# Performance work log

Hardware: AMD Instinct MI355X
Metric: run time of the kernel (lower is better)

## Reference

```python
import jax, jax.numpy as jnp
import numpy as np

EPS = 1e-5
NEG = -1.0e9

def ln(x, g, b):
    m = x.mean(-1, keepdims=True)
    v = ((x - m) ** 2).mean(-1, keepdims=True)
    return (x - m) * jax.lax.rsqrt(v + EPS) * g + b

def setup_inputs() -> dict:
    B, N, DH, DE, H = 2, 512, 256, 64, 8
    key = jax.random.key(0)
    ks = jax.random.split(key, 8)
    s = 0.02
    f32 = jnp.float32
    return {
        'h': jax.random.normal(ks[0], (B, N, DH), f32),
        'e': jax.random.normal(ks[1], (B, N, N, DE), f32),
        'mask': jnp.ones((B, N), f32),
        'Wqkv': jax.random.normal(ks[2], (DH, 3 * DH), f32) * s,
        'bqkv': jnp.zeros((3 * DH,), f32),
        'Wout': jax.random.normal(ks[3], (DH, DH), f32) * s,
        'bout': jnp.zeros((DH,), f32),
        'Web': jax.random.normal(ks[4], (DE, H), f32) * s,
        'beb': jnp.zeros((H,), f32),
        'eb_g': jnp.ones((H,), f32), 'eb_b': jnp.zeros((H,), f32),
        'W1': jax.random.normal(ks[5], (2 * DH + DE, DE), f32) * s,
        'b1': jnp.zeros((DE,), f32),
        'mlp_g': jnp.ones((DE,), f32), 'mlp_b': jnp.zeros((DE,), f32),
        'W2': jax.random.normal(ks[6], (DE, DE), f32) * s,
        'b2': jnp.zeros((DE,), f32),
        'nh_g': jnp.ones((DH,), f32), 'nh_b': jnp.zeros((DH,), f32),
        'ne_g': jnp.ones((DE,), f32), 'ne_b': jnp.zeros((DE,), f32),
    }

def reference(h, e, mask, Wqkv, bqkv, Wout, bout, Web, beb, eb_g, eb_b,
              W1, b1, mlp_g, mlp_b, W2, b2, nh_g, nh_b, ne_g, ne_b):
    B, N, DH = h.shape
    DE = e.shape[-1]
    H = Web.shape[-1]
    dh = DH // H
    # additive pad mask: [B,N,N] -> broadcast over heads
    pad = (1.0 - mask) * NEG                  # [B,N]
    attn_mask = (pad[:, :, None] + pad[:, None, :])[:, None]  # [B,1,N,N]
    h_res = h
    hn = ln(h, nh_g, nh_b)
    qkv = hn @ Wqkv + bqkv                    # [B,N,3*DH]
    q, k, v = jnp.split(qkv, 3, axis=-1)
    q = q.reshape(B, N, H, dh)
    k = k.reshape(B, N, H, dh)
    v = v.reshape(B, N, H, dh)
    en = ln(e, ne_g, ne_b)                    # [B,N,N,DE]
    edge_bias = ln(en @ Web + beb, eb_g, eb_b)  # [B,N,N,H]
    edge_bias = jnp.transpose(edge_bias, (0, 3, 1, 2))  # [B,H,N,N]
    scores = jnp.einsum('bihd,bjhd->bhij', q, k) / np.sqrt(dh).astype(np.float32)
    probs = jax.nn.softmax(scores + edge_bias + attn_mask, axis=-1)
    h_out = jnp.einsum('bhij,bjhd->bihd', probs, v).reshape(B, N, DH)
    h_out = h_out @ Wout + bout
    h_new = h_res + h_out                     # dropout p=0 (eval)
    # pairwise edge update
    h_i = jnp.broadcast_to(h_new[:, :, None, :], (B, N, N, DH))
    h_j = jnp.broadcast_to(h_new[:, None, :, :], (B, N, N, DH))
    e_in = jnp.concatenate([h_i, h_j, en], axis=-1)  # [B,N,N,2*DH+DE]
    e_out = ln(jax.nn.relu(e_in @ W1 + b1), mlp_g, mlp_b) @ W2 + b2
    e_new = e + e_out
    return (h_new, e_new)
```

## Files before the change

### kernel.cpp

```cpp
#include <hip/hip_runtime.h>
#include <math.h>

#define BB 2
#define NN 512
#define DH 256
#define DE 64
#define NH 8
#define EPS 1e-5f
#define NEGV (-1.0e9f)

__global__ __launch_bounds__(256) void k1_ln_qkv(
    const float* __restrict__ h, const float* __restrict__ nh_g,
    const float* __restrict__ nh_b, const float* __restrict__ Wqkv,
    const float* __restrict__ bqkv, float* __restrict__ q,
    float* __restrict__ k, float* __restrict__ vt)
{
    __shared__ float hn[4][DH];
    const int tid = threadIdx.x;
    const int wave = tid >> 6, lane = tid & 63;
    const int row0 = blockIdx.x * 4;
    const int row = row0 + wave;

    float x[4];
    float s = 0.f, ss = 0.f;
#pragma unroll
    for (int jj = 0; jj < 4; jj++) {
        x[jj] = h[(size_t)row * DH + lane + 64 * jj];
        s += x[jj]; ss += x[jj] * x[jj];
    }
#pragma unroll
    for (int m = 32; m >= 1; m >>= 1) { s += __shfl_xor(s, m); ss += __shfl_xor(ss, m); }
    const float mean = s * (1.0f / DH);
    const float var = ss * (1.0f / DH) - mean * mean;
    const float rstd = rsqrtf(var + EPS);
#pragma unroll
    for (int jj = 0; jj < 4; jj++) {
        const int c = lane + 64 * jj;
        hn[wave][c] = (x[jj] - mean) * rstd * nh_g[c] + nh_b[c];
    }
    __syncthreads();

    float acc[4][3];
#pragma unroll
    for (int r = 0; r < 4; r++) {
        acc[r][0] = bqkv[tid];
        acc[r][1] = bqkv[tid + 256];
        acc[r][2] = bqkv[tid + 512];
    }
    for (int kk = 0; kk < DH; kk++) {
        const float w0 = Wqkv[(size_t)kk * 768 + tid];
        const float w1 = Wqkv[(size_t)kk * 768 + tid + 256];
        const float w2 = Wqkv[(size_t)kk * 768 + tid + 512];
#pragma unroll
        for (int r = 0; r < 4; r++) {
            const float hv = hn[r][kk];
            acc[r][0] += hv * w0; acc[r][1] += hv * w1; acc[r][2] += hv * w2;
        }
    }
    const float qscale = 0.17677669529663687f;
    const int hh = tid >> 5, d = tid & 31;
#pragma unroll
    for (int r = 0; r < 4; r++) {
        const int rw = row0 + r;
        const int b = rw >> 9, i = rw & 511;
        q[(((size_t)(b * NH + hh) * NN) + i) * 32 + d] = acc[r][0] * qscale;
        k[(((size_t)(b * NH + hh) * NN) + i) * 32 + d] = acc[r][1];
        vt[(((size_t)(b * NH + hh) * 32) + d) * NN + i] = acc[r][2];
    }
}

__global__ __launch_bounds__(256) void k2_edge_bias(
    const float* __restrict__ e, const float* __restrict__ Web,
    const float* __restrict__ beb, const float* __restrict__ eb_g,
    const float* __restrict__ eb_b, const float* __restrict__ ne_g,
    const float* __restrict__ ne_b, float* __restrict__ ebias)
{
    __shared__ float tile[4][64][65];
    const int wave = threadIdx.x >> 6, lane = threadIdx.x & 63;
    const int t = blockIdx.x * 4 + wave;
    const int j0 = (t & 7) * 64;
    const int bi = t >> 3;
    const int b = bi >> 9, i = bi & 511;

    const float* src = e + ((size_t)bi * NN + j0) * DE;
#pragma unroll
    for (int it = 0; it < 16; it++) {
        const int f = it * 256 + lane * 4;
        const float4 v = *(const float4*)(src + f);
        const int r = f >> 6, c = f & 63;
        tile[wave][r][c] = v.x; tile[wave][r][c + 1] = v.y;
        tile[wave][r][c + 2] = v.z; tile[wave][r][c + 3] = v.w;
    }
    __syncthreads();

    float s = 0.f, ss = 0.f;
    for (int d = 0; d < 64; d++) {
        const float x = tile[wave][lane][d];
        s += x; ss += x * x;
    }
    const float mean = s * (1.0f / 64), var = ss * (1.0f / 64) - mean * mean;
    const float rstd = rsqrtf(var + EPS);

    float acc[8];
#pragma unroll
    for (int hh = 0; hh < 8; hh++) acc[hh] = beb[hh];
    for (int d = 0; d < 64; d++) {
        const float x = tile[wave][lane][d];
        const float en = (x - mean) * rstd * ne_g[d] + ne_b[d];
#pragma unroll
        for (int hh = 0; hh < 8; hh++) acc[hh] += en * Web[d * 8 + hh];
    }
    float s2 = 0.f, ss2 = 0.f;
#pragma unroll
    for (int hh = 0; hh < 8; hh++) { s2 += acc[hh]; ss2 += acc[hh] * acc[hh]; }
    const float m2 = s2 * 0.125f, v2 = ss2 * 0.125f - m2 * m2;
    const float r2 = rsqrtf(v2 + EPS);
#pragma unroll
    for (int hh = 0; hh < 8; hh++) {
        const float v = (acc[hh] - m2) * r2 * eb_g[hh] + eb_b[hh];
        ebias[(((size_t)(b * NH + hh) * NN) + i) * NN + j0 + lane] = v;
    }
}

__global__ __launch_bounds__(256) void k3a_softmax(
    const float* __restrict__ q, const float* __restrict__ k,
    const float* __restrict__ mask, float* __restrict__ ebias)
{
    const int bh = blockIdx.x >> 9;
    const int i = blockIdx.x & 511;
    const int b = bh >> 3;
    const int tid = threadIdx.x;
    const int wave = tid >> 6, lane = tid & 63;

    __shared__ __align__(16) float qrow[32];
    __shared__ float red[4];
    if (tid < 32) qrow[tid] = q[((size_t)bh * NN + i) * 32 + tid];
    __syncthreads();

    const float pad_i = (1.0f - mask[b * NN + i]) * NEGV;
    float sv[2];
#pragma unroll
    for (int u = 0; u < 2; u++) {
        const int j = tid + u * 256;
        const float4* kr = (const float4*)(k + ((size_t)bh * NN + j) * 32);
        float a = 0.f;
#pragma unroll
        for (int d4 = 0; d4 < 8; d4++) {
            const float4 kv = kr[d4];
            const float4 qv = *(const float4*)(qrow + d4 * 4);
            a += kv.x * qv.x + kv.y * qv.y + kv.z * qv.z + kv.w * qv.w;
        }
        const float pad_j = (1.0f - mask[b * NN + j]) * NEGV;
        sv[u] = a + ebias[(((size_t)bh * NN) + i) * NN + j] + pad_i + pad_j;
    }
    float mx = fmaxf(sv[0], sv[1]);
#pragma unroll
    for (int m = 32; m >= 1; m >>= 1) mx = fmaxf(mx, __shfl_xor(mx, m));
    if (lane == 0) red[wave] = mx;
    __syncthreads();
    mx = fmaxf(fmaxf(red[0], red[1]), fmaxf(red[2], red[3]));
    __syncthreads();
    const float p0 = __expf(sv[0] - mx), p1 = __expf(sv[1] - mx);
    float sm = p0 + p1;
#pragma unroll
    for (int m = 32; m >= 1; m >>= 1) sm += __shfl_xor(sm, m);
    if (lane == 0) red[wave] = sm;
    __syncthreads();
    const float inv = 1.0f / (red[0] + red[1] + red[2] + red[3]);
    ebias[(((size_t)bh * NN) + i) * NN + tid] = p0 * inv;
    ebias[(((size_t)bh * NN) + i) * NN + tid + 256] = p1 * inv;
}

__global__ __launch_bounds__(256) void k3b_av_out(
    const float* __restrict__ probs, const float* __restrict__ vt,
    const float* __restrict__ h, const float* __restrict__ Wout,
    const float* __restrict__ bout, float* __restrict__ hnew)
{
    const int bi = blockIdx.x;
    const int b = bi >> 9, i = bi & 511;
    const int tid = threadIdx.x;
    __shared__ __align__(16) float p[NH * NN];
    __shared__ float ao[DH];
#pragma unroll
    for (int it = 0; it < 16; it++) {
        const int f = it * 256 + tid;
        const int hh = f >> 9, j = f & 511;
        p[f] = probs[(((size_t)(b * NH + hh) * NN) + i) * NN + j];
    }
    __syncthreads();
    const int hh = tid >> 5, d = tid & 31;
    const float* vrow = vt + (((size_t)(b * NH + hh) * 32) + d) * NN;
    float a = 0.f;
    for (int j4 = 0; j4 < 128; j4++) {
        const float4 vv = *(const float4*)(vrow + j4 * 4);
        const float4 pv = *(const float4*)(&p[hh * NN + j4 * 4]);
        a += vv.x * pv.x + vv.y * pv.y + vv.z * pv.z + vv.w * pv.w;
    }
    ao[tid] = a;
    __syncthreads();
    float out = bout[tid];
    for (int kk = 0; kk < DH; kk++) out += ao[kk] * Wout[(size_t)kk * DH + tid];
    hnew[(size_t)bi * DH + tid] = h[(size_t)bi * DH + tid] + out;
}

__global__ __launch_bounds__(64) void k4_hw1(
    const float* __restrict__ hnew, const float* __restrict__ W1,
    const float* __restrict__ b1, float* __restrict__ hW1a,
    float* __restrict__ hW1b)
{
    const int row = blockIdx.x;
    const int c = threadIdx.x;
    __shared__ float hr[DH];
#pragma unroll
    for (int t = 0; t < 4; t++) hr[c + 64 * t] = hnew[(size_t)row * DH + c + 64 * t];
    __syncthreads();
    float a = b1[c], bb = 0.f;
    for (int kk = 0; kk < DH; kk++) {
        const float hv = hr[kk];
        a += hv * W1[(size_t)kk * 64 + c];
        bb += hv * W1[(size_t)(256 + kk) * 64 + c];
    }
    hW1a[(size_t)row * 64 + c] = a;
    hW1b[(size_t)row * 64 + c] = bb;
}

__global__ __launch_bounds__(256) void k5_edge_mlp(
    const float* __restrict__ e, const float* __restrict__ ne_g,
    const float* __restrict__ ne_b, const float* __restrict__ W1c,
    const float* __restrict__ hW1a, const float* __restrict__ hW1b,
    const float* __restrict__ mlp_g, const float* __restrict__ mlp_b,
    const float* __restrict__ W2, const float* __restrict__ b2,
    float* __restrict__ enew)
{
    __shared__ float tile[4][64][65];
    const int wave = threadIdx.x >> 6, lane = threadIdx.x & 63;
    const int t = blockIdx.x * 4 + wave;
    const int j0 = (t & 7) * 64;
    const int bi = t >> 3;
    const int b = bi >> 9;

    const float* src = e + ((size_t)bi * NN + j0) * DE;
#pragma unroll
    for (int it = 0; it < 16; it++) {
        const int f = it * 256 + lane * 4;
        const float4 v = *(const float4*)(src + f);
        const int r = f >> 6, c = f & 63;
        tile[wave][r][c] = v.x; tile[wave][r][c + 1] = v.y;
        tile[wave][r][c + 2] = v.z; tile[wave][r][c + 3] = v.w;
    }
    __syncthreads();

    float s = 0.f, ss = 0.f;
    for (int d = 0; d < 64; d++) {
        const float x = tile[wave][lane][d];
        s += x; ss += x * x;
    }
    const float mean = s * (1.0f / 64), var = ss * (1.0f / 64) - mean * mean;
    const float rstd = rsqrtf(var + EPS);
    for (int d = 0; d < 64; d++) {
        const float x = tile[wave][lane][d];
        tile[wave][lane][d] = (x - mean) * rstd * ne_g[d] + ne_b[d];
    }

    const float* hA = hW1a + (size_t)bi * 64;
    const float* hB = hW1b + ((size_t)(b * NN + j0 + lane)) * 64;
    float acc[64];
#pragma unroll
    for (int c4 = 0; c4 < 16; c4++) {
        const float4 ha = *(const float4*)(hA + c4 * 4);
        const float4 hb = *(const float4*)(hB + c4 * 4);
        acc[c4 * 4 + 0] = ha.x + hb.x; acc[c4 * 4 + 1] = ha.y + hb.y;
        acc[c4 * 4 + 2] = ha.z + hb.z; acc[c4 * 4 + 3] = ha.w + hb.w;
    }
    for (int d = 0; d < 64; d++) {
        const float en = tile[wave][lane][d];
        const float* w = W1c + (size_t)d * 64;
#pragma unroll
        for (int c = 0; c < 64; c++) acc[c] += en * w[c];
    }
    float s2 = 0.f, ss2 = 0.f;
#pragma unroll
    for (int c = 0; c < 64; c++) {
        acc[c] = fmaxf(acc[c], 0.f);
        s2 += acc[c]; ss2 += acc[c] * acc[c];
    }
    const float m2 = s2 * (1.0f / 64), v2 = ss2 * (1.0f / 64) - m2 * m2;
    const float r2 = rsqrtf(v2 + EPS);
#pragma unroll
    for (int c = 0; c < 64; c++)
        tile[wave][lane][c] = (acc[c] - m2) * r2 * mlp_g[c] + mlp_b[c];
#pragma unroll
    for (int c = 0; c < 64; c++) acc[c] = b2[c];
    for (int d = 0; d < 64; d++) {
        const float u = tile[wave][lane][d];
        const float* w = W2 + (size_t)d * 64;
#pragma unroll
        for (int c = 0; c < 64; c++) acc[c] += u * w[c];
    }
    const float* erow = e + (((size_t)bi * NN) + j0 + lane) * DE;
    float* drow = enew + (((size_t)bi * NN) + j0 + lane) * DE;
#pragma unroll
    for (int c4 = 0; c4 < 16; c4++) {
        const float4 ev = *(const float4*)(erow + c4 * 4);
        float4 o;
        o.x = acc[c4 * 4 + 0] + ev.x; o.y = acc[c4 * 4 + 1] + ev.y;
        o.z = acc[c4 * 4 + 2] + ev.z; o.w = acc[c4 * 4 + 3] + ev.w;
        *(float4*)(drow + c4 * 4) = o;
    }
}

extern "C" void kernel_launch(void* const* d_in, const int* in_sizes, int n_in,
                              void* d_out, int out_size, void* d_ws, size_t ws_size,
                              hipStream_t stream)
{
    const float* h    = (const float*)d_in[0];
    const float* e    = (const float*)d_in[1];
    const float* mask = (const float*)d_in[2];
    const float* Wqkv = (const float*)d_in[3];
    const float* bqkv = (const float*)d_in[4];
    const float* Wout = (const float*)d_in[5];
    const float* bout = (const float*)d_in[6];
    const float* Web  = (const float*)d_in[7];
    const float* beb  = (const float*)d_in[8];
    const float* eb_g = (const float*)d_in[9];
    const float* eb_b = (const float*)d_in[10];
    const float* W1   = (const float*)d_in[11];
    const float* b1   = (const float*)d_in[12];
    const float* mlp_g= (const float*)d_in[13];
    const float* mlp_b= (const float*)d_in[14];
    const float* W2   = (const float*)d_in[15];
    const float* b2   = (const float*)d_in[16];
    const float* nh_g = (const float*)d_in[17];
    const float* nh_b = (const float*)d_in[18];
    const float* ne_g = (const float*)d_in[19];
    const float* ne_b = (const float*)d_in[20];

    float* ws   = (float*)d_ws;
    float* q    = ws;
    float* kbuf = ws + 262144;
    float* vt   = ws + 524288;
    float* eb   = ws + 786432;
    float* hW1a = ws + 786432 + 4194304;
    float* hW1b = hW1a + 65536;

    float* hnew = (float*)d_out;
    float* enew = hnew + 262144;

    hipLaunchKernelGGL(k1_ln_qkv, dim3(256), dim3(256), 0, stream,
                       h, nh_g, nh_b, Wqkv, bqkv, q, kbuf, vt);
    hipLaunchKernelGGL(k2_edge_bias, dim3(2048), dim3(256), 0, stream,
                       e, Web, beb, eb_g, eb_b, ne_g, ne_b, eb);
    hipLaunchKernelGGL(k3a_softmax, dim3(8192), dim3(256), 0, stream,
                       q, kbuf, mask, eb);
    hipLaunchKernelGGL(k3b_av_out, dim3(1024), dim3(256), 0, stream,
                       eb, vt, h, Wout, bout, hnew);
    hipLaunchKernelGGL(k4_hw1, dim3(1024), dim3(64), 0, stream,
                       hnew, W1, b1, hW1a, hW1b);
    hipLaunchKernelGGL(k5_edge_mlp, dim3(2048), dim3(256), 0, stream,
                       e, ne_g, ne_b, W1 + 512 * 64, hW1a, hW1b,
                       mlp_g, mlp_b, W2, b2, enew);
}
```

Before: 687.3 us.

## Drop LDS edge tiles; read edge rows directly per thread and keep MLP in registers

The edge-bias and edge-MLP kernels no longer stage the 64-wide edge rows through a padded shared-memory tile. Each thread now reads its own row straight from global memory with float4 loads, twice (once for LayerNorm statistics, once for the projection), and the second MLP layer runs in two 32-column halves from register-resident activations instead of going through LDS. The output projection in the attention kernel is also split into four independent accumulators to shorten the dependency chain. Per-thread row loads are strided 256 bytes apart across lanes, so coalescing is worse and the edge tensor is read more times, with reliance on cache to absorb the repeats. Register pressure may also rise.

```diff
diff --git a/kernel.cpp b/kernel.cpp
--- a/kernel.cpp
+++ b/kernel.cpp
@@ -75,28 +75,18 @@
     const float* __restrict__ eb_b, const float* __restrict__ ne_g,
     const float* __restrict__ ne_b, float* __restrict__ ebias)
 {
-    __shared__ float tile[4][64][65];
-    const int wave = threadIdx.x >> 6, lane = threadIdx.x & 63;
-    const int t = blockIdx.x * 4 + wave;
-    const int j0 = (t & 7) * 64;
-    const int bi = t >> 3;
-    const int b = bi >> 9, i = bi & 511;
-
-    const float* src = e + ((size_t)bi * NN + j0) * DE;
-#pragma unroll
-    for (int it = 0; it < 16; it++) {
-        const int f = it * 256 + lane * 4;
-        const float4 v = *(const float4*)(src + f);
-        const int r = f >> 6, c = f & 63;
-        tile[wave][r][c] = v.x; tile[wave][r][c + 1] = v.y;
-        tile[wave][r][c + 2] = v.z; tile[wave][r][c + 3] = v.w;
-    }
-    __syncthreads();
+    const int idx = blockIdx.x * 256 + threadIdx.x;
+    const int b = idx >> 18;
+    const int i = (idx >> 9) & 511;
+    const int j = idx & 511;
+    const float4* erow = (const float4*)(e + (size_t)idx * DE);
 
     float s = 0.f, ss = 0.f;
-    for (int d = 0; d < 64; d++) {
-        const float x = tile[wave][lane][d];
-        s += x; ss += x * x;
+#pragma unroll 1
+    for (int d4 = 0; d4 < 16; d4++) {
+        const float4 v = erow[d4];
+        s += v.x + v.y + v.z + v.w;
+        ss += v.x * v.x + v.y * v.y + v.z * v.z + v.w * v.w;
     }
     const float mean = s * (1.0f / 64), var = ss * (1.0f / 64) - mean * mean;
     const float rstd = rsqrtf(var + EPS);
@@ -104,11 +94,20 @@
     float acc[8];
 #pragma unroll
     for (int hh = 0; hh < 8; hh++) acc[hh] = beb[hh];
-    for (int d = 0; d < 64; d++) {
-        const float x = tile[wave][lane][d];
-        const float en = (x - mean) * rstd * ne_g[d] + ne_b[d];
-#pragma unroll
-        for (int hh = 0; hh < 8; hh++) acc[hh] += en * Web[d * 8 + hh];
+#pragma unroll 1
+    for (int d4 = 0; d4 < 16; d4++) {
+        const float4 v = erow[d4];
+        float en[4];
+        en[0] = (v.x - mean) * rstd * ne_g[d4 * 4 + 0] + ne_b[d4 * 4 + 0];
+        en[1] = (v.y - mean) * rstd * ne_g[d4 * 4 + 1] + ne_b[d4 * 4 + 1];
+        en[2] = (v.z - mean) * rstd * ne_g[d4 * 4 + 2] + ne_b[d4 * 4 + 2];
+        en[3] = (v.w - mean) * rstd * ne_g[d4 * 4 + 3] + ne_b[d4 * 4 + 3];
+#pragma unroll
+        for (int t = 0; t < 4; t++) {
+            const float* w = Web + (d4 * 4 + t) * 8;
+#pragma unroll
+            for (int hh = 0; hh < 8; hh++) acc[hh] += en[t] * w[hh];
+        }
     }
     float s2 = 0.f, ss2 = 0.f;
 #pragma unroll
@@ -118,7 +117,7 @@
 #pragma unroll
     for (int hh = 0; hh < 8; hh++) {
         const float v = (acc[hh] - m2) * r2 * eb_g[hh] + eb_b[hh];
-        ebias[(((size_t)(b * NH + hh) * NN) + i) * NN + j0 + lane] = v;
+        ebias[(((size_t)(b * NH + hh) * NN) + i) * NN + j] = v;
     }
 }
 
@@ -198,9 +197,15 @@
     }
     ao[tid] = a;
     __syncthreads();
-    float out = bout[tid];
-    for (int kk = 0; kk < DH; kk++) out += ao[kk] * Wout[(size_t)kk * DH + tid];
-    hnew[(size_t)bi * DH + tid] = h[(size_t)bi * DH + tid] + out;
+    float o0 = 0.f, o1 = 0.f, o2 = 0.f, o3 = 0.f;
+    for (int kk = 0; kk < DH; kk += 4) {
+        o0 += ao[kk + 0] * Wout[(size_t)(kk + 0) * DH + tid];
+        o1 += ao[kk + 1] * Wout[(size_t)(kk + 1) * DH + tid];
+        o2 += ao[kk + 2] * Wout[(size_t)(kk + 2) * DH + tid];
+        o3 += ao[kk + 3] * Wout[(size_t)(kk + 3) * DH + tid];
+    }
+    hnew[(size_t)bi * DH + tid] =
+        h[(size_t)bi * DH + tid] + bout[tid] + ((o0 + o1) + (o2 + o3));
 }
 
 __global__ __launch_bounds__(64) void k4_hw1(
@@ -232,38 +237,24 @@
     const float* __restrict__ W2, const float* __restrict__ b2,
     float* __restrict__ enew)
 {
-    __shared__ float tile[4][64][65];
-    const int wave = threadIdx.x >> 6, lane = threadIdx.x & 63;
-    const int t = blockIdx.x * 4 + wave;
-    const int j0 = (t & 7) * 64;
-    const int bi = t >> 3;
-    const int b = bi >> 9;
-
-    const float* src = e + ((size_t)bi * NN + j0) * DE;
-#pragma unroll
-    for (int it = 0; it < 16; it++) {
-        const int f = it * 256 + lane * 4;
-        const float4 v = *(const float4*)(src + f);
-        const int r = f >> 6, c = f & 63;
-        tile[wave][r][c] = v.x; tile[wave][r][c + 1] = v.y;
-        tile[wave][r][c + 2] = v.z; tile[wave][r][c + 3] = v.w;
-    }
-    __syncthreads();
+    const int idx = blockIdx.x * 256 + threadIdx.x;
+    const int b = idx >> 18;
+    const int j = idx & 511;
+    const int bi = idx >> 9;
+    const float4* erow = (const float4*)(e + (size_t)idx * DE);
 
     float s = 0.f, ss = 0.f;
-    for (int d = 0; d < 64; d++) {
-        const float x = tile[wave][lane][d];
-        s += x; ss += x * x;
+#pragma unroll 1
+    for (int d4 = 0; d4 < 16; d4++) {
+        const float4 v = erow[d4];
+        s += v.x + v.y + v.z + v.w;
+        ss += v.x * v.x + v.y * v.y + v.z * v.z + v.w * v.w;
     }
     const float mean = s * (1.0f / 64), var = ss * (1.0f / 64) - mean * mean;
     const float rstd = rsqrtf(var + EPS);
-    for (int d = 0; d < 64; d++) {
-        const float x = tile[wave][lane][d];
-        tile[wave][lane][d] = (x - mean) * rstd * ne_g[d] + ne_b[d];
-    }
 
     const float* hA = hW1a + (size_t)bi * 64;
-    const float* hB = hW1b + ((size_t)(b * NN + j0 + lane)) * 64;
+    const float* hB = hW1b + ((size_t)(b * NN + j)) * 64;
     float acc[64];
 #pragma unroll
     for (int c4 = 0; c4 < 16; c4++) {
@@ -272,12 +263,23 @@
         acc[c4 * 4 + 0] = ha.x + hb.x; acc[c4 * 4 + 1] = ha.y + hb.y;
         acc[c4 * 4 + 2] = ha.z + hb.z; acc[c4 * 4 + 3] = ha.w + hb.w;
     }
-    for (int d = 0; d < 64; d++) {
-        const float en = tile[wave][lane][d];
-        const float* w = W1c + (size_t)d * 64;
-#pragma unroll
-        for (int c = 0; c < 64; c++) acc[c] += en * w[c];
-    }
+
+#pragma unroll 1
+    for (int d4 = 0; d4 < 16; d4++) {
+        const float4 v = erow[d4];
+        float en[4];
+        en[0] = (v.x - mean) * rstd * ne_g[d4 * 4 + 0] + ne_b[d4 * 4 + 0];
+        en[1] = (v.y - mean) * rstd * ne_g[d4 * 4 + 1] + ne_b[d4 * 4 + 1];
+        en[2] = (v.z - mean) * rstd * ne_g[d4 * 4 + 2] + ne_b[d4 * 4 + 2];
+        en[3] = (v.w - mean) * rstd * ne_g[d4 * 4 + 3] + ne_b[d4 * 4 + 3];
+#pragma unroll
+        for (int t = 0; t < 4; t++) {
+            const float* w = W1c + (size_t)(d4 * 4 + t) * 64;
+#pragma unroll
+            for (int c = 0; c < 64; c++) acc[c] += en[t] * w[c];
+        }
+    }
+
     float s2 = 0.f, ss2 = 0.f;
 #pragma unroll
     for (int c = 0; c < 64; c++) {
@@ -288,24 +290,30 @@
     const float r2 = rsqrtf(v2 + EPS);
 #pragma unroll
     for (int c = 0; c < 64; c++)
-        tile[wave][lane][c] = (acc[c] - m2) * r2 * mlp_g[c] + mlp_b[c];
-#pragma unroll
-    for (int c = 0; c < 64; c++) acc[c] = b2[c];
-    for (int d = 0; d < 64; d++) {
-        const float u = tile[wave][lane][d];
-        const float* w = W2 + (size_t)d * 64;
-#pragma unroll
-        for (int c = 0; c < 64; c++) acc[c] += u * w[c];
-    }
-    const float* erow = e + (((size_t)bi * NN) + j0 + lane) * DE;
-    float* drow = enew + (((size_t)bi * NN) + j0 + lane) * DE;
-#pragma unroll
-    for (int c4 = 0; c4 < 16; c4++) {
-        const float4 ev = *(const float4*)(erow + c4 * 4);
-        float4 o;
-        o.x = acc[c4 * 4 + 0] + ev.x; o.y = acc[c4 * 4 + 1] + ev.y;
-        o.z = acc[c4 * 4 + 2] + ev.z; o.w = acc[c4 * 4 + 3] + ev.w;
-        *(float4*)(drow + c4 * 4) = o;
+        acc[c] = (acc[c] - m2) * r2 * mlp_g[c] + mlp_b[c];
+
+    const float* erowf = e + (size_t)idx * 64;
+    float* drow = enew + (size_t)idx * 64;
+#pragma unroll
+    for (int half = 0; half < 2; half++) {
+        float outc[32];
+#pragma unroll
+        for (int c = 0; c < 32; c++) outc[c] = b2[half * 32 + c];
+#pragma unroll
+        for (int d = 0; d < 64; d++) {
+            const float u = acc[d];
+            const float* w = W2 + (size_t)d * 64 + half * 32;
+#pragma unroll
+            for (int c = 0; c < 32; c++) outc[c] += u * w[c];
+        }
+#pragma unroll
+        for (int c4 = 0; c4 < 8; c4++) {
+            const float4 ev = *(const float4*)(erowf + half * 32 + c4 * 4);
+            float4 o;
+            o.x = outc[c4 * 4 + 0] + ev.x; o.y = outc[c4 * 4 + 1] + ev.y;
+            o.z = outc[c4 * 4 + 2] + ev.z; o.w = outc[c4 * 4 + 3] + ev.w;
+            *(float4*)(drow + half * 32 + c4 * 4) = o;
+        }
     }
 }
 
```

Measured after the change: 960.5 us. 1.4x slower.
